# Kernel optimization log

Hardware: AMD Instinct MI355X
Metric: run time of the kernel (lower is better)

The kernel has to match this reference:

```python
import jax, jax.numpy as jnp
import numpy as np

WS = 14      # window size
NH = 12      # num heads
LN_EPS = 1e-3  # keras LayerNormalization default epsilon


def _ln(x, scale, bias):
    mu = jnp.mean(x, axis=-1, keepdims=True)
    var = jnp.mean(jnp.square(x - mu), axis=-1, keepdims=True)
    return (x - mu) * jax.lax.rsqrt(var + LN_EPS) * scale + bias


def setup_inputs() -> dict:
    key = jax.random.key(0)
    ks = jax.random.split(key, 8)
    B, H, W, C = 4, 64, 64, 768
    hd = C // NH
    s = 0.02
    f32 = jnp.float32
    return {
        "x": jax.random.normal(ks[0], (B, H, W, C), f32),
        "ln1_scale": jnp.ones((C,), f32), "ln1_bias": jnp.zeros((C,), f32),
        "wqkv": (jax.random.normal(ks[1], (C, 3 * C), f32) * s), "bqkv": jnp.zeros((3 * C,), f32),
        "wproj": (jax.random.normal(ks[2], (C, C), f32) * s), "bproj": jnp.zeros((C,), f32),
        "rel_pos_h": jax.random.normal(ks[3], (2 * WS - 1, hd), f32) * s,
        "rel_pos_w": jax.random.normal(ks[4], (2 * WS - 1, hd), f32) * s,
        "ln2_scale": jnp.ones((C,), f32), "ln2_bias": jnp.zeros((C,), f32),
        "w1": (jax.random.normal(ks[5], (C, 4 * C), f32) * s), "b1": jnp.zeros((4 * C,), f32),
        "w2": (jax.random.normal(ks[6], (4 * C, C), f32) * s), "b2": jnp.zeros((C,), f32),
    }


def reference(x, ln1_scale, ln1_bias, wqkv, bqkv, wproj, bproj,
              rel_pos_h, rel_pos_w, ln2_scale, ln2_bias, w1, b1, w2, b2):
    B, H, W, C = x.shape
    hd = C // NH
    ws = WS
    shortcut = x
    x = _ln(x, ln1_scale, ln1_bias)

    # ---- window partition (pad to multiple of ws) ----
    pad_h = (ws - H % ws) % ws
    pad_w = (ws - W % ws) % ws
    x = jnp.pad(x, ((0, 0), (0, pad_h), (0, pad_w), (0, 0)))
    Hp, Wp = H + pad_h, W + pad_w
    nwh, nww = Hp // ws, Wp // ws
    xw = x.reshape(B, nwh, ws, nww, ws, C).transpose(0, 1, 3, 2, 4, 5)
    xw = xw.reshape(B * nwh * nww, ws, ws, C)  # [Bw, ws, ws, C]
    Bw, N = xw.shape[0], ws * ws

    # ---- relative positional multi-head attention ----
    qkv = (xw.reshape(Bw, N, C) @ wqkv + bqkv).reshape(Bw, N, 3, NH, hd)
    q, k, v = jnp.moveaxis(qkv, 2, 0)                 # each [Bw, N, NH, hd]
    q = q.transpose(0, 2, 1, 3)                       # [Bw, NH, N, hd]
    k = k.transpose(0, 2, 1, 3)
    v = v.transpose(0, 2, 1, 3)
    scale = hd ** -0.5
    attn = jnp.einsum('bhqd,bhkd->bhqk', q * scale, k)  # [Bw, NH, N, N]

    # decomposed rel-pos bias (q_size == k_size == ws, no interpolation)
    rel = jnp.arange(ws)[:, None] - jnp.arange(ws)[None, :] + (ws - 1)
    Rh = rel_pos_h[rel]  # [ws, ws, hd]
    Rw = rel_pos_w[rel]  # [ws, ws, hd]
    rq = q.reshape(Bw, NH, ws, ws, hd)                 # unscaled q, as in SAM
    rel_h = jnp.einsum('bnhwc,hkc->bnhwk', rq, Rh)     # [Bw, NH, ws, ws, ws(kh)]
    rel_w = jnp.einsum('bnhwc,wkc->bnhwk', rq, Rw)     # [Bw, NH, ws, ws, ws(kw)]
    attn = (attn.reshape(Bw, NH, ws, ws, ws, ws)
            + rel_h[:, :, :, :, :, None]
            + rel_w[:, :, :, :, None, :]).reshape(Bw, NH, N, N)

    attn = jax.nn.softmax(attn, axis=-1)
    out = jnp.einsum('bhqk,bhkd->bhqd', attn, v)       # [Bw, NH, N, hd]
    out = out.transpose(0, 2, 1, 3).reshape(Bw, ws, ws, C)
    out = out @ wproj + bproj

    # ---- window unpartition (crop padding) ----
    out = out.reshape(B, nwh, nww, ws, ws, C).transpose(0, 1, 3, 2, 4, 5)
    out = out.reshape(B, Hp, Wp, C)[:, :H, :W, :]

    x = shortcut + out
    # ---- MLP block (Linear -> exact GELU -> Linear), keras gelu approximate=False
    h = jax.nn.gelu(_ln(x, ln2_scale, ln2_bias) @ w1 + b1, approximate=False)
    return x + (h @ w2 + b2)
```

## Files before the change

kernel.cpp:

```cpp
#include <hip/hip_runtime.h>

typedef unsigned short u16;
typedef unsigned int u32;
typedef __attribute__((ext_vector_type(8))) __bf16 bf16x8;
typedef __attribute__((ext_vector_type(8))) unsigned short u16x8;
typedef __attribute__((ext_vector_type(4))) float f32x4;
typedef __attribute__((ext_vector_type(16))) float f32x16;
typedef __attribute__((ext_vector_type(4))) unsigned int u32x4;

#define BATCH 4
#define IMGH 64
#define IMGW 64
#define CH 768
#define NWIN 100
#define NTOK 196
#define NHEAD 12
#define HD 64
#define MVALID 19600
#define MPAD 19712
#define QKVSZ 15052800
#define VTPAD 224
#define MLPCHUNK 4096

__device__ __forceinline__ float bl(u32 u) { return __builtin_bit_cast(float, u << 16); }
__device__ __forceinline__ float bh(u32 u) { return __builtin_bit_cast(float, u & 0xffff0000u); }
__device__ __forceinline__ u16 f2b(float f) {
    u32 u = __builtin_bit_cast(u32, f);
    u += 0x7fffu + ((u >> 16) & 1u);
    return (u16)(u >> 16);
}
__device__ __forceinline__ float wredsum(float v) {
#pragma unroll
    for (int off = 32; off >= 1; off >>= 1) v += __shfl_xor(v, off);
    return v;
}
__device__ __forceinline__ float bsel(u32 pk, int kd) {
    return (kd & 1) ? __builtin_bit_cast(float, pk & 0xffff0000u)
                    : __builtin_bit_cast(float, pk << 16);
}
__device__ __forceinline__ u32 cvtpk(float lo, float hi) {
    u32 r;
    asm("v_cvt_pk_bf16_f32 %0, %1, %2" : "=v"(r) : "v"(lo), "v"(hi));
    return r;
}

#define GLOAD16(g, l) __builtin_amdgcn_global_load_lds( \
    (const __attribute__((address_space(1))) unsigned int*)(g), \
    (__attribute__((address_space(3))) unsigned int*)(l), 16, 0, 0)

__global__ __launch_bounds__(256) void transpose_cast(const float* __restrict__ in,
                                                      u16* __restrict__ outp, int R, int C) {
    __shared__ float tile[32][33];
    int tx = threadIdx.x & 31, ty = threadIdx.x >> 5;
    int bc = blockIdx.x * 32, br = blockIdx.y * 32;
#pragma unroll
    for (int i = ty; i < 32; i += 8) tile[i][tx] = in[(size_t)(br + i) * C + bc + tx];
    __syncthreads();
#pragma unroll
    for (int i = ty; i < 32; i += 8) outp[(size_t)(bc + i) * R + br + tx] = f2b(tile[tx][i]);
}

__global__ __launch_bounds__(256) void ln_part_kernel(const float* __restrict__ x,
                                                      const float* __restrict__ sc,
                                                      const float* __restrict__ bi,
                                                      u16* __restrict__ Xw) {
    int row = blockIdx.x, tid = threadIdx.x;
    u16* orow = Xw + (size_t)row * CH;
    int wwin = row / NTOK, nn = row % NTOK;
    int b = wwin / 25, wrem = wwin % 25;
    int wh = wrem / 5, ww = wrem % 5;
    int ii = nn / 14, jj = nn % 14;
    int h = wh * 14 + ii, w = ww * 14 + jj;
    if (row >= MVALID || h >= IMGH || w >= IMGW) {
#pragma unroll
        for (int t = 0; t < 3; ++t) orow[tid + 256 * t] = 0;
        return;
    }
    const float* xr = x + (((size_t)b * IMGH + h) * IMGW + w) * CH;
    float v0 = xr[tid], v1 = xr[tid + 256], v2 = xr[tid + 512];
    float s = wredsum(v0 + v1 + v2);
    __shared__ float red[4], red2[4];
    if ((tid & 63) == 0) red[tid >> 6] = s;
    __syncthreads();
    float mean = (red[0] + red[1] + red[2] + red[3]) * (1.f / 768.f);
    float d0 = v0 - mean, d1 = v1 - mean, d2 = v2 - mean;
    float q = wredsum(d0 * d0 + d1 * d1 + d2 * d2);
    if ((tid & 63) == 0) red2[tid >> 6] = q;
    __syncthreads();
    float var = (red2[0] + red2[1] + red2[2] + red2[3]) * (1.f / 768.f);
    float rstd = rsqrtf(var + 1e-3f);
    orow[tid]       = f2b(d0 * rstd * sc[tid]       + bi[tid]);
    orow[tid + 256] = f2b(d1 * rstd * sc[tid + 256] + bi[tid + 256]);
    orow[tid + 512] = f2b(d2 * rstd * sc[tid + 512] + bi[tid + 512]);
}

__global__ __launch_bounds__(256) void ln2_kernel(const float* __restrict__ xin,
                                                  const float* __restrict__ sc,
                                                  const float* __restrict__ bi,
                                                  u16* __restrict__ outp) {
    int row = blockIdx.x, tid = threadIdx.x;
    const float* xr = xin + (size_t)row * CH;
    float v0 = xr[tid], v1 = xr[tid + 256], v2 = xr[tid + 512];
    float s = wredsum(v0 + v1 + v2);
    __shared__ float red[4], red2[4];
    if ((tid & 63) == 0) red[tid >> 6] = s;
    __syncthreads();
    float mean = (red[0] + red[1] + red[2] + red[3]) * (1.f / 768.f);
    float d0 = v0 - mean, d1 = v1 - mean, d2 = v2 - mean;
    float q = wredsum(d0 * d0 + d1 * d1 + d2 * d2);
    if ((tid & 63) == 0) red2[tid >> 6] = q;
    __syncthreads();
    float var = (red2[0] + red2[1] + red2[2] + red2[3]) * (1.f / 768.f);
    float rstd = rsqrtf(var + 1e-3f);
    u16* orow = outp + (size_t)row * CH;
    orow[tid]       = f2b(d0 * rstd * sc[tid]       + bi[tid]);
    orow[tid + 256] = f2b(d1 * rstd * sc[tid + 256] + bi[tid + 256]);
    orow[tid + 512] = f2b(d2 * rstd * sc[tid + 512] + bi[tid + 512]);
}

template <int EPI>
__global__ __launch_bounds__(256) void gemm_bt(const u16* __restrict__ A,
                                               const u16* __restrict__ Bt,
                                               const float* __restrict__ bias,
                                               void* __restrict__ Cout,
                                               const float* __restrict__ extra,
                                               int K) {
    __shared__ u16 As[4096];
    __shared__ u16 Bs[4096];
    int tid = threadIdx.x, lane = tid & 63, wave = tid >> 6;
    int bm = blockIdx.x, bn = blockIdx.y;
    int wr = wave >> 1, wc = wave & 1;
    int fr = lane & 15, fk = lane >> 4;
    f32x4 acc[4][4] = {};
    const u16* Ag = A + (size_t)bm * 128 * K;
    const u16* Bg = Bt + (size_t)bn * 128 * K;
    int arow0 = (wave * 2) * 16 + (lane >> 2);
    int arow1 = arow0 + 16;
    int acol = (lane & 3) * 8;
    for (int k0 = 0; k0 < K; k0 += 32) {
        GLOAD16(Ag + (size_t)arow0 * K + k0 + acol, As + wave * 1024);
        GLOAD16(Ag + (size_t)arow1 * K + k0 + acol, As + wave * 1024 + 512);
        GLOAD16(Bg + (size_t)arow0 * K + k0 + acol, Bs + wave * 1024);
        GLOAD16(Bg + (size_t)arow1 * K + k0 + acol, Bs + wave * 1024 + 512);
        __syncthreads();
        const u16x8* Asv = (const u16x8*)As;
        const u16x8* Bsv = (const u16x8*)Bs;
        bf16x8 a[4], b[4];
#pragma unroll
        for (int m = 0; m < 4; ++m)
            a[m] = __builtin_bit_cast(bf16x8, Asv[(wr * 64 + m * 16 + fr) * 4 + fk]);
#pragma unroll
        for (int n = 0; n < 4; ++n)
            b[n] = __builtin_bit_cast(bf16x8, Bsv[(wc * 64 + n * 16 + fr) * 4 + fk]);
#pragma unroll
        for (int m = 0; m < 4; ++m)
#pragma unroll
            for (int n = 0; n < 4; ++n)
                acc[m][n] = __builtin_amdgcn_mfma_f32_16x16x32_bf16(a[m], b[n], acc[m][n], 0, 0, 0);
        __syncthreads();
    }
#pragma unroll
    for (int n = 0; n < 4; ++n) {
        int gcol = bn * 128 + wc * 64 + n * 16 + fr;
        float bv = bias[gcol];
        if constexpr (EPI == 0) {
            int which = gcol / 768, rem = gcol % 768;
            int head = rem >> 6, c = rem & 63;
            if (which == 2) {
#pragma unroll
                for (int m = 0; m < 4; ++m) {
                    int growb = bm * 128 + wr * 64 + m * 16 + fk * 4;
                    if (growb < MVALID) {
                        int wwin = growb / NTOK, nn = growb % NTOK;
                        int np = (nn & ~12) | ((nn & 4) << 1) | ((nn & 8) >> 1);
                        size_t idx = 2 * (size_t)QKVSZ + ((((size_t)wwin * NHEAD + head) * HD + c) * VTPAD + np);
                        uint2 d;
                        d.x = (u32)f2b(acc[m][n][0] + bv) | ((u32)f2b(acc[m][n][1] + bv) << 16);
                        d.y = (u32)f2b(acc[m][n][2] + bv) | ((u32)f2b(acc[m][n][3] + bv) << 16);
                        *(uint2*)((u16*)Cout + idx) = d;
                    }
                }
            } else {
#pragma unroll
                for (int m = 0; m < 4; ++m) {
                    int growb = bm * 128 + wr * 64 + m * 16 + fk * 4;
#pragma unroll
                    for (int j = 0; j < 4; ++j) {
                        int grow = growb + j;
                        if (grow < MVALID) {
                            int wwin = grow / NTOK, nn = grow % NTOK;
                            size_t idx = ((((size_t)which * NWIN + wwin) * NHEAD + head) * NTOK + nn) * HD + c;
                            ((u16*)Cout)[idx] = f2b(acc[m][n][j] + bv);
                        }
                    }
                }
            }
        } else if constexpr (EPI == 1) {
#pragma unroll
            for (int m = 0; m < 4; ++m) {
                int growb = bm * 128 + wr * 64 + m * 16 + fk * 4;
#pragma unroll
                for (int j = 0; j < 4; ++j) {
                    int grow = growb + j;
                    if (grow < MVALID) {
                        int wwin = grow / NTOK, nn = grow % NTOK;
                        int b_ = wwin / 25, wrem = wwin % 25;
                        int wh = wrem / 5, ww = wrem % 5;
                        int ii = nn / 14, jj = nn % 14;
                        int h = wh * 14 + ii, w = ww * 14 + jj;
                        if (h < IMGH && w < IMGW) {
                            size_t idx = (((size_t)b_ * IMGH + h) * IMGW + w) * CH + gcol;
                            ((float*)Cout)[idx] = extra[idx] + acc[m][n][j] + bv;
                        }
                    }
                }
            }
        } else if constexpr (EPI == 2) {
#pragma unroll
            for (int m = 0; m < 4; ++m) {
                int growb = bm * 128 + wr * 64 + m * 16 + fk * 4;
#pragma unroll
                for (int j = 0; j < 4; ++j) {
                    int grow = growb + j;
                    float v = acc[m][n][j] + bv;
                    float g = 0.5f * v * (1.f + erff(v * 0.70710678118654752f));
                    ((u16*)Cout)[(size_t)grow * 3072 + gcol] = f2b(g);
                }
            }
        } else {
#pragma unroll
            for (int m = 0; m < 4; ++m) {
                int growb = bm * 128 + wr * 64 + m * 16 + fk * 4;
#pragma unroll
                for (int j = 0; j < 4; ++j) {
                    int grow = growb + j;
                    size_t idx = (size_t)grow * CH + gcol;
                    ((float*)Cout)[idx] = extra[idx] + acc[m][n][j] + bv;
                }
            }
        }
    }
}

#define DIV14(x) (((x) * 4682) >> 16)

__global__ __launch_bounds__(448, 4) void attn_kernel(const u16* __restrict__ qkv,
                                                      const float* __restrict__ rph,
                                                      const float* __restrict__ rpw,
                                                      u16* __restrict__ aout) {
    __shared__ __align__(16) u16 Vt[64 * 256];
    __shared__ u16 tblH[7][960];
    __shared__ u16 tblW[7][960];
    __shared__ float linvs[7][32];
    int tid = threadIdx.x, lane = tid & 63, wv = tid >> 6;
    int blk = blockIdx.x;
    int win = blk / NHEAD, head = blk % NHEAD;
    const u16* Qg = qkv + (size_t)blk * (NTOK * HD);
    const u16* Kg = qkv + QKVSZ + (size_t)blk * (NTOK * HD);
    const u16* VTg = qkv + 2 * (size_t)QKVSZ + (size_t)blk * (HD * VTPAD);

    for (int u = tid; u < 1792; u += 448) {
        int c = u / 28, s = u - c * 28;
        uint4 d = ((const uint4*)VTg)[u];
        *(uint4*)((char*)Vt + c * 512 + (((s + c) & 31) << 4)) = d;
    }
    __syncthreads();

    int l31 = lane & 31, h = lane >> 5;
    int qt = wv;
    int q = qt * 32 + l31;
    int qe = q > 195 ? 195 : q;
    int qi = DIV14(qe), qj = qe - qi * 14;

    bf16x8 qf[4];
    {
        const u16* qrow = Qg + qe * HD + 8 * h;
#pragma unroll
        for (int ks = 0; ks < 4; ++ks)
            qf[ks] = __builtin_bit_cast(bf16x8, *(const u16x8*)(qrow + ks * 16));
    }
    {
        f32x16 aH = {}, aW = {};
        int rr = l31 > 26 ? 26 : l31;
        const float* ph = rph + rr * 64 + 8 * h;
        const float* pw = rpw + rr * 64 + 8 * h;
#pragma unroll
        for (int ks = 0; ks < 4; ++ks) {
            u16x8 va, vb;
#pragma unroll
            for (int e = 0; e < 8; ++e) { va[e] = f2b(ph[ks * 16 + e]); vb[e] = f2b(pw[ks * 16 + e]); }
            aH = __builtin_amdgcn_mfma_f32_32x32x16_bf16(__builtin_bit_cast(bf16x8, va), qf[ks], aH, 0, 0, 0);
            aW = __builtin_amdgcn_mfma_f32_32x32x16_bf16(__builtin_bit_cast(bf16x8, vb), qf[ks], aW, 0, 0, 0);
        }
        u16* th = tblH[wv]; u16* tw = tblW[wv];
#pragma unroll
        for (int i = 0; i < 8; ++i) {
            int R = ((2 * i) & 3) + 8 * ((2 * i) >> 2);
            int rel = R + 4 * h;
            if (rel < 28) {
                *(u32*)&th[l31 * 30 + rel] = cvtpk(aH[2 * i], aH[2 * i + 1]);
                *(u32*)&tw[l31 * 30 + rel] = cvtpk(aW[2 * i], aW[2 * i + 1]);
            }
        }
    }
    u32 BH[7], BW[7];
    {
        const u16* th = tblH[wv]; const u16* tw = tblW[wv];
#pragma unroll
        for (int i = 0; i < 7; ++i) {
            u32 a0 = th[l31 * 30 + (qi + 13 - 2 * i)];
            u32 a1 = th[l31 * 30 + (qi + 12 - 2 * i)];
            BH[i] = a0 | (a1 << 16);
            u32 b0 = tw[l31 * 30 + (qj + 13 - 2 * i)];
            u32 b1 = tw[l31 * 30 + (qj + 12 - 2 * i)];
            BW[i] = b0 | (b1 << 16);
        }
    }

    f32x16 acc0 = {}, acc1 = {};
    float lsum = 0.f;
#pragma unroll
    for (int kt = 0; kt < 7; ++kt) {
        f32x16 S = {};
        {
            int krow = kt * 32 + l31; if (krow > 195) krow = 195;
            const u16* kp = Kg + krow * HD + 8 * h;
#pragma unroll
            for (int ks = 0; ks < 4; ++ks) {
                bf16x8 ka = __builtin_bit_cast(bf16x8, *(const u16x8*)(kp + ks * 16));
                S = __builtin_amdgcn_mfma_f32_32x32x16_bf16(ka, qf[ks], S, 0, 0, 0);
            }
        }
        float p[16];
#pragma unroll
        for (int r = 0; r < 16; ++r) {
            int R = (r & 3) + 8 * (r >> 2);
            if (kt == 6 && R >= 4) { p[r] = 0.f; continue; }
            int k0 = kt * 32 + R;
            int kd0 = k0 / 14, kj0 = k0 - kd0 * 14;
            float bhv, bwv;
            if (kt == 6) {
                bhv = bsel(BH[kd0 >> 1], kd0);
                bwv = bsel(BW[kj0 >> 1], kj0);
            } else {
                int k1 = k0 + 4;
                int kd1 = k1 / 14, kj1 = k1 - kd1 * 14;
                bhv = h ? bsel(BH[kd1 >> 1], kd1) : bsel(BH[kd0 >> 1], kd0);
                bwv = h ? bsel(BW[kj1 >> 1], kj1) : bsel(BW[kj0 >> 1], kj0);
            }
            float s = fminf(S[r] * 0.125f + bhv + bwv, 30.f);
            float pe = __expf(s);
            if (kt == 6) pe = h ? 0.f : pe;
            p[r] = pe;
            lsum += pe;
        }
        u32 cw[8];
#pragma unroll
        for (int i = 0; i < 8; ++i) cw[i] = cvtpk(p[2 * i], p[2 * i + 1]);
#pragma unroll
        for (int ks = 0; ks < 2; ++ks) {
            u32x4 paw = {cw[ks * 4 + 0], cw[ks * 4 + 1], cw[ks * 4 + 2], cw[ks * 4 + 3]};
            bf16x8 pa = __builtin_bit_cast(bf16x8, paw);
            int slot = kt * 4 + ks * 2 + h;
            bf16x8 v0 = __builtin_bit_cast(bf16x8,
                *(const u16x8*)((char*)Vt + l31 * 512 + (((slot + l31) & 31) << 4)));
            bf16x8 v1 = __builtin_bit_cast(bf16x8,
                *(const u16x8*)((char*)Vt + (32 + l31) * 512 + (((slot + 32 + l31) & 31) << 4)));
            acc0 = __builtin_amdgcn_mfma_f32_32x32x16_bf16(pa, v0, acc0, 0, 0, 0);
            acc1 = __builtin_amdgcn_mfma_f32_32x32x16_bf16(pa, v1, acc1, 0, 0, 0);
        }
    }
    lsum += __shfl_xor(lsum, 32);
    if (h == 0) linvs[wv][l31] = 1.f / lsum;
#pragma unroll
    for (int r = 0; r < 16; ++r) {
        int R = (r & 3) + 8 * (r >> 2);
        int qq = qt * 32 + R + 4 * h;
        if (qq < 196) {
            float li = linvs[wv][R + 4 * h];
            size_t base = (size_t)(win * NTOK + qq) * CH + head * HD + l31;
            aout[base]      = f2b(acc0[r] * li);
            aout[base + 32] = f2b(acc1[r] * li);
        }
    }
}

extern "C" void kernel_launch(void* const* d_in, const int* in_sizes, int n_in,
                              void* d_out, int out_size, void* d_ws, size_t ws_size,
                              hipStream_t stream) {
    const float* x     = (const float*)d_in[0];
    const float* ln1_s = (const float*)d_in[1];
    const float* ln1_b = (const float*)d_in[2];
    const float* wqkv  = (const float*)d_in[3];
    const float* bqkv  = (const float*)d_in[4];
    const float* wproj = (const float*)d_in[5];
    const float* bproj = (const float*)d_in[6];
    const float* rph   = (const float*)d_in[7];
    const float* rpw   = (const float*)d_in[8];
    const float* ln2_s = (const float*)d_in[9];
    const float* ln2_b = (const float*)d_in[10];
    const float* w1    = (const float*)d_in[11];
    const float* b1    = (const float*)d_in[12];
    const float* w2    = (const float*)d_in[13];
    const float* b2    = (const float*)d_in[14];

    char* ws = (char*)d_ws;
    size_t off = 0;
    auto alloc = [&](size_t bytes) { char* p = ws + off; off += (bytes + 255) & ~(size_t)255; return p; };
    u16* WqkvT  = (u16*)alloc((size_t)2304 * 768 * 2);
    u16* WprojT = (u16*)alloc((size_t)768 * 768 * 2);
    u16* W1T    = (u16*)alloc((size_t)3072 * 768 * 2);
    u16* W2T    = (u16*)alloc((size_t)768 * 3072 * 2);
    char* XWREG = alloc((size_t)MPAD * CH * 2);
    char* BIG   = alloc((size_t)2 * QKVSZ * 2 + (size_t)NWIN * NHEAD * HD * VTPAD * 2);
    u16*   Xw       = (u16*)XWREG;
    u16*   attn_out = (u16*)XWREG;
    u16*   x2ln     = (u16*)XWREG;
    u16*   qkvb     = (u16*)BIG;
    float* x2       = (float*)BIG;
    u16*   hbuf     = (u16*)(BIG + (size_t)52800000);

    dim3 blk(256);
    transpose_cast<<<dim3(2304 / 32, 768 / 32), blk, 0, stream>>>(wqkv, WqkvT, 768, 2304);
    transpose_cast<<<dim3(768 / 32, 768 / 32),  blk, 0, stream>>>(wproj, WprojT, 768, 768);
    transpose_cast<<<dim3(3072 / 32, 768 / 32), blk, 0, stream>>>(w1, W1T, 768, 3072);
    transpose_cast<<<dim3(768 / 32, 3072 / 32), blk, 0, stream>>>(w2, W2T, 3072, 768);

    ln_part_kernel<<<MPAD, blk, 0, stream>>>(x, ln1_s, ln1_b, Xw);

    gemm_bt<0><<<dim3(MPAD / 128, 2304 / 128), blk, 0, stream>>>(Xw, WqkvT, bqkv, qkvb, nullptr, 768);

    attn_kernel<<<NWIN * NHEAD, dim3(448), 0, stream>>>(qkvb, rph, rpw, attn_out);

    gemm_bt<1><<<dim3(MPAD / 128, 768 / 128), blk, 0, stream>>>(attn_out, WprojT, bproj, x2, x, 768);

    ln2_kernel<<<16384, blk, 0, stream>>>(x2, ln2_s, ln2_b, x2ln);

    for (int c = 0; c < 16384 / MLPCHUNK; ++c) {
        const u16* aln = x2ln + (size_t)c * MLPCHUNK * CH;
        gemm_bt<2><<<dim3(MLPCHUNK / 128, 3072 / 128), blk, 0, stream>>>(aln, W1T, b1, hbuf, nullptr, 768);
        float* outc = (float*)d_out + (size_t)c * MLPCHUNK * CH;
        const float* x2c = x2 + (size_t)c * MLPCHUNK * CH;
        gemm_bt<3><<<dim3(MLPCHUNK / 128, 768 / 128), blk, 0, stream>>>(hbuf, W2T, b2, outc, x2c, 3072);
    }
}
```

Measured before the change: 909.4 us.

## Swizzle GEMM block order into 8-row panels and enlarge MLP chunk size

Replaces the 2D GEMM grid with a 1D grid remapped so groups of 8 M-tiles sweep across all N-tiles together. This is meant to improve L2 reuse of the A panel and weight tiles. It also sizes the MLP chunk to the available workspace, up to all 16384 rows, which cuts kernel launches and gives each launch a larger grid. In exchange it depends on ws_size being large enough and on the hidden buffer fitting after the BIG region.

```diff
diff --git a/kernel.cpp b/kernel.cpp
--- a/kernel.cpp
+++ b/kernel.cpp
@@ -20,7 +20,6 @@
 #define MPAD 19712
 #define QKVSZ 15052800
 #define VTPAD 224
-#define MLPCHUNK 4096
 
 __device__ __forceinline__ float bl(u32 u) { return __builtin_bit_cast(float, u << 16); }
 __device__ __forceinline__ float bh(u32 u) { return __builtin_bit_cast(float, u & 0xffff0000u); }
@@ -124,11 +123,25 @@
                                                const float* __restrict__ bias,
                                                void* __restrict__ Cout,
                                                const float* __restrict__ extra,
-                                               int K) {
+                                               int K, int nbm, int nbn) {
     __shared__ u16 As[4096];
     __shared__ u16 Bs[4096];
     int tid = threadIdx.x, lane = tid & 63, wave = tid >> 6;
-    int bm = blockIdx.x, bn = blockIdx.y;
+    int bid = blockIdx.x;
+    int fullp = nbm >> 3;
+    int fullBlocks = fullp * 8 * nbn;
+    int bm, bn;
+    if (bid < fullBlocks) {
+        int panel = bid / (8 * nbn);
+        int rem = bid - panel * 8 * nbn;
+        bm = panel * 8 + (rem & 7);
+        bn = rem >> 3;
+    } else {
+        int rem = bid - fullBlocks;
+        int tb = nbm - fullp * 8;
+        bm = fullp * 8 + rem % tb;
+        bn = rem / tb;
+    }
     int wr = wave >> 1, wc = wave & 1;
     int fr = lane & 15, fk = lane >> 4;
     f32x4 acc[4][4] = {};
@@ -412,7 +425,8 @@
     u16* W1T    = (u16*)alloc((size_t)3072 * 768 * 2);
     u16* W2T    = (u16*)alloc((size_t)768 * 3072 * 2);
     char* XWREG = alloc((size_t)MPAD * CH * 2);
-    char* BIG   = alloc((size_t)2 * QKVSZ * 2 + (size_t)NWIN * NHEAD * HD * VTPAD * 2);
+    char* BIG   = ws + off;
+    size_t bigAvail = (ws_size > off) ? (ws_size - off) : 0;
     u16*   Xw       = (u16*)XWREG;
     u16*   attn_out = (u16*)XWREG;
     u16*   x2ln     = (u16*)XWREG;
@@ -420,6 +434,11 @@
     float* x2       = (float*)BIG;
     u16*   hbuf     = (u16*)(BIG + (size_t)52800000);
 
+    int MCH;
+    if (bigAvail >= (size_t)52800000 + (size_t)16384 * 3072 * 2)      MCH = 16384;
+    else if (bigAvail >= (size_t)52800000 + (size_t)8192 * 3072 * 2)  MCH = 8192;
+    else                                                              MCH = 4096;
+
     dim3 blk(256);
     transpose_cast<<<dim3(2304 / 32, 768 / 32), blk, 0, stream>>>(wqkv, WqkvT, 768, 2304);
     transpose_cast<<<dim3(768 / 32, 768 / 32),  blk, 0, stream>>>(wproj, WprojT, 768, 768);
@@ -428,19 +447,20 @@
 
     ln_part_kernel<<<MPAD, blk, 0, stream>>>(x, ln1_s, ln1_b, Xw);
 
-    gemm_bt<0><<<dim3(MPAD / 128, 2304 / 128), blk, 0, stream>>>(Xw, WqkvT, bqkv, qkvb, nullptr, 768);
+    gemm_bt<0><<<dim3(154 * 18), blk, 0, stream>>>(Xw, WqkvT, bqkv, qkvb, nullptr, 768, 154, 18);
 
     attn_kernel<<<NWIN * NHEAD, dim3(448), 0, stream>>>(qkvb, rph, rpw, attn_out);
 
-    gemm_bt<1><<<dim3(MPAD / 128, 768 / 128), blk, 0, stream>>>(attn_out, WprojT, bproj, x2, x, 768);
+    gemm_bt<1><<<dim3(154 * 6), blk, 0, stream>>>(attn_out, WprojT, bproj, x2, x, 768, 154, 6);
 
     ln2_kernel<<<16384, blk, 0, stream>>>(x2, ln2_s, ln2_b, x2ln);
 
-    for (int c = 0; c < 16384 / MLPCHUNK; ++c) {
-        const u16* aln = x2ln + (size_t)c * MLPCHUNK * CH;
-        gemm_bt<2><<<dim3(MLPCHUNK / 128, 3072 / 128), blk, 0, stream>>>(aln, W1T, b1, hbuf, nullptr, 768);
-        float* outc = (float*)d_out + (size_t)c * MLPCHUNK * CH;
-        const float* x2c = x2 + (size_t)c * MLPCHUNK * CH;
-        gemm_bt<3><<<dim3(MLPCHUNK / 128, 768 / 128), blk, 0, stream>>>(hbuf, W2T, b2, outc, x2c, 3072);
-    }
-}
+    int nbmC = MCH / 128;
+    for (int c = 0; c < 16384 / MCH; ++c) {
+        const u16* aln = x2ln + (size_t)c * MCH * CH;
+        gemm_bt<2><<<dim3(nbmC * 24), blk, 0, stream>>>(aln, W1T, b1, hbuf, nullptr, 768, nbmC, 24);
+        float* outc = (float*)d_out + (size_t)c * MCH * CH;
+        const float* x2c = x2 + (size_t)c * MCH * CH;
+        gemm_bt<3><<<dim3(nbmC * 6), blk, 0, stream>>>(hbuf, W2T, b2, outc, x2c, 3072, nbmC, 6);
+    }
+}
```

Result: faster. 773.2 us (-15.0%).
